# Kernel optimization log

Hardware: AMD Instinct MI355X
Metric: run time of the kernel (lower is better)

## Reference

```python
import jax, jax.numpy as jnp
import numpy as np

V = 50257; E = 1024; H = 1024; L = 256; NL = 2; D = 10


def setup_inputs() -> dict:
    key = jax.random.key(0)
    ks = jax.random.split(key, 16)
    n = lambda k, s: jax.random.normal(k, s, dtype=jnp.float32)
    return {
        "input_tok": jax.random.randint(ks[0], (1, 1), 0, V),
        "h0": n(ks[1], (NL, 1, H)),
        "c0": n(ks[2], (NL, 1, H)),
        "h_s": n(ks[3], (L, 1, H)),
        "h_t_tilde": n(ks[4], (1, 1, H)),
        "emb": n(ks[5], (V, E)) * 0.02,
        "Wp": n(ks[6], (H, H)) * (H ** -0.5),
        "wdot": n(ks[7], (1, H)) * (H ** -0.5),
        "Wbil": n(ks[8], (1, H, H)) * (H ** -0.5),
        "Wcomb": n(ks[9], (H, 2 * H)) * ((2 * H) ** -0.5),
        "bcomb": jnp.zeros((H,), jnp.float32),
        "Wih0": n(ks[10], (4 * H, E + H)) * ((E + H) ** -0.5),
        "Whh0": n(ks[11], (4 * H, H)) * (H ** -0.5),
        "bih0": jnp.zeros((4 * H,), jnp.float32),
        "bhh0": jnp.zeros((4 * H,), jnp.float32),
        "Wih1": n(ks[12], (4 * H, H)) * (H ** -0.5),
        "Whh1": n(ks[13], (4 * H, H)) * (H ** -0.5),
        "bih1": jnp.zeros((4 * H,), jnp.float32),
        "bhh1": jnp.zeros((4 * H,), jnp.float32),
        "Wout": n(ks[14], (V, H)) * (H ** -0.5),
        "bout": jnp.zeros((V,), jnp.float32),
    }


def _lstm_cell(x, h, c, Wih, Whh, bih, bhh):
    # torch LSTM gate order: i, f, g, o
    g = x @ Wih.T + bih + h @ Whh.T + bhh
    i, f, gg, o = jnp.split(g, 4, axis=-1)
    c2 = jax.nn.sigmoid(f) * c + jax.nn.sigmoid(i) * jnp.tanh(gg)
    h2 = jax.nn.sigmoid(o) * jnp.tanh(c2)
    return h2, c2


def reference(input_tok, h0, c0, h_s, h_t_tilde, emb, Wp, wdot, Wbil, Wcomb, bcomb,
              Wih0, Whh0, bih0, bhh0, Wih1, Whh1, bih1, bhh1, Wout, bout):
    embedding = emb[input_tok]                                  # [1,1,E]
    x = jnp.concatenate((embedding, h_t_tilde), axis=-1)[0]     # [1,E+H]
    h1, c1 = _lstm_cell(x, h0[0], c0[0], Wih0, Whh0, bih0, bhh0)
    h2, c2 = _lstm_cell(h1, h0[1], c0[1], Wih1, Whh1, bih1, bhh1)
    h_new = jnp.stack((h1, h2)); c_new = jnp.stack((c1, c2))
    h_t = h2                                                    # [1,H]
    Ls = h_s.shape[0]
    p_t = Ls * jax.nn.sigmoid(jnp.tanh(h_t @ Wp.T) @ wdot.T).squeeze()  # scalar
    s = jnp.round(p_t).astype(jnp.int32)
    idx = jnp.arange(Ls)
    lo = jnp.maximum(s - D, 0); hi = jnp.minimum(s + D, Ls - 1)
    mask = (idx >= lo) & (idx <= hi)                            # [L] local window
    # bilinear score h_t^T W h_s over all positions; mask outside window
    score = jnp.einsum('bh,ohk,lbk->lbo', h_t, Wbil, h_s)       # [L,1,1]
    neg = jnp.finfo(score.dtype).min
    a = jax.nn.softmax(jnp.where(mask[:, None, None], score, neg), axis=0)
    # NOTE: original uses exp(+d^2/(D/2)^2) (no minus sign); replicated faithfully.
    expo = jnp.where(mask, ((idx.astype(jnp.float32) - p_t) ** 2) / ((D / 2) ** 2), 0.0)
    a_t = a * jnp.exp(expo)[:, None, None]                      # [L,1,1]
    win = (hi - lo + 1).astype(jnp.float32)
    context = jnp.sum(a_t * h_s, axis=0, keepdims=True) / win   # [1,1,H] (mean over window)
    cat = jnp.concatenate((context, h_t[None]), axis=-1)        # [1,1,2H]
    h_t_tilde_new = jnp.tanh(cat @ Wcomb.T + bcomb)             # [1,1,H]
    y = jax.nn.log_softmax(h_t_tilde_new @ Wout.T + bout, axis=-1)  # [1,1,V]
    return (y, h_new, c_new, h_t_tilde_new, a_t, p_t)
```

## Files before the change

kernel.cpp:

```cpp
#include <hip/hip_runtime.h>
#include <math.h>

#define V 50257
#define E 1024
#define HH 1024
#define LL 256

#define O_H  (V)
#define O_C  (V + 2*HH)
#define O_HT (V + 4*HH)
#define O_A  (V + 5*HH)
#define O_P  (V + 5*HH + LL)

#define W_T    0
#define W_V    1024
#define W_CTX  2304
#define W_Z    4096
#define W_BM   54400
#define W_BS   55424

#define NB_LOGITS 786

__device__ __forceinline__ float sigmoidf_(float x) { return 1.f / (1.f + expf(-x)); }
__device__ __forceinline__ float dot4(float4 a, float4 b) {
    return a.x * b.x + a.y * b.y + a.z * b.z + a.w * b.w;
}

__device__ __forceinline__ float block_sum(float v, float* red) {
    int lane = threadIdx.x & 63, wv = threadIdx.x >> 6;
#pragma unroll
    for (int o = 32; o > 0; o >>= 1) v += __shfl_down(v, o, 64);
    if (lane == 0) red[wv] = v;
    __syncthreads();
    return red[0] + red[1] + red[2] + red[3];
}

__global__ void k_lstm(const float* __restrict__ Wih, const float* __restrict__ Whh,
                       const float* __restrict__ bih, const float* __restrict__ bhh,
                       const float* __restrict__ xa_base, const int* __restrict__ tok,
                       const float* __restrict__ xb, int na, int nb,
                       const float* __restrict__ hprev, const float* __restrict__ cprev,
                       float* __restrict__ hout, float* __restrict__ cout,
                       float* __restrict__ zero_buf) {
    const int u = blockIdx.x;
    const int K = na + nb;
    const int K4 = K >> 2, na4 = na >> 2;
    if (zero_buf && threadIdx.x == 0) zero_buf[u] = 0.f;
    const float* xa = tok ? (xa_base + (size_t)tok[0] * na) : xa_base;
    const float4* xa4 = (const float4*)xa;
    const float4* xb4 = (const float4*)xb;
    const float4* r0 = (const float4*)(Wih + (size_t)u * K);
    const float4* r1 = (const float4*)(Wih + (size_t)(u + HH) * K);
    const float4* r2 = (const float4*)(Wih + (size_t)(u + 2*HH) * K);
    const float4* r3 = (const float4*)(Wih + (size_t)(u + 3*HH) * K);
    float a0 = 0, a1 = 0, a2 = 0, a3 = 0;
    for (int j = threadIdx.x; j < K4; j += 256) {
        float4 xv = (j < na4) ? xa4[j] : xb4[j - na4];
        a0 += dot4(r0[j], xv); a1 += dot4(r1[j], xv);
        a2 += dot4(r2[j], xv); a3 += dot4(r3[j], xv);
    }
    const float4* s0 = (const float4*)(Whh + (size_t)u * HH);
    const float4* s1 = (const float4*)(Whh + (size_t)(u + HH) * HH);
    const float4* s2 = (const float4*)(Whh + (size_t)(u + 2*HH) * HH);
    const float4* s3 = (const float4*)(Whh + (size_t)(u + 3*HH) * HH);
    const float4* hp4 = (const float4*)hprev;
    {
        int j = threadIdx.x;
        float4 hv = hp4[j];
        a0 += dot4(s0[j], hv); a1 += dot4(s1[j], hv);
        a2 += dot4(s2[j], hv); a3 += dot4(s3[j], hv);
    }
    int lane = threadIdx.x & 63, wv = threadIdx.x >> 6;
#pragma unroll
    for (int o = 32; o > 0; o >>= 1) {
        a0 += __shfl_down(a0, o, 64);
        a1 += __shfl_down(a1, o, 64);
        a2 += __shfl_down(a2, o, 64);
        a3 += __shfl_down(a3, o, 64);
    }
    __shared__ float sm[4][4];
    if (lane == 0) { sm[wv][0] = a0; sm[wv][1] = a1; sm[wv][2] = a2; sm[wv][3] = a3; }
    __syncthreads();
    if (threadIdx.x == 0) {
        float gi = sm[0][0]+sm[1][0]+sm[2][0]+sm[3][0] + bih[u]        + bhh[u];
        float gf = sm[0][1]+sm[1][1]+sm[2][1]+sm[3][1] + bih[u+HH]     + bhh[u+HH];
        float gg = sm[0][2]+sm[1][2]+sm[2][2]+sm[3][2] + bih[u+2*HH]   + bhh[u+2*HH];
        float go = sm[0][3]+sm[1][3]+sm[2][3]+sm[3][3] + bih[u+3*HH]   + bhh[u+3*HH];
        float c = sigmoidf_(gf) * cprev[u] + sigmoidf_(gi) * tanhf(gg);
        hout[u] = sigmoidf_(go) * tanhf(c);
        cout[u] = c;
    }
}

__global__ void k_ptv(const float* __restrict__ Wp, const float* __restrict__ Wbil,
                      const float* __restrict__ h2, float* __restrict__ t_out,
                      float* __restrict__ v_out) {
    __shared__ float red[4];
    if (blockIdx.x < HH) {
        int r = blockIdx.x;
        const float4* row = (const float4*)(Wp + (size_t)r * HH);
        const float4* h24 = (const float4*)h2;
        float acc = dot4(row[threadIdx.x], h24[threadIdx.x]);
        float tot = block_sum(acc, red);
        if (threadIdx.x == 0) t_out[r] = tanhf(tot);
    } else {
        int b = blockIdx.x - HH;
        int h0 = b * 32;
        int k4 = threadIdx.x;
        const float4* W4 = (const float4*)Wbil;
        float4 acc = make_float4(0.f, 0.f, 0.f, 0.f);
        for (int h = h0; h < h0 + 32; ++h) {
            float hv = h2[h];
            float4 w = W4[(size_t)h * 256 + k4];
            acc.x += hv * w.x; acc.y += hv * w.y;
            acc.z += hv * w.z; acc.w += hv * w.w;
        }
        atomicAdd(&v_out[k4 * 4 + 0], acc.x);
        atomicAdd(&v_out[k4 * 4 + 1], acc.y);
        atomicAdd(&v_out[k4 * 4 + 2], acc.z);
        atomicAdd(&v_out[k4 * 4 + 3], acc.w);
    }
}

__global__ void k_attn(const float* __restrict__ wdot, const float* __restrict__ t,
                       const float* __restrict__ v, const float* __restrict__ hs,
                       float* __restrict__ ctx, float* __restrict__ a_out,
                       float* __restrict__ pt_out) {
    const int tid = threadIdx.x;
    const int lane = tid & 63, wv = tid >> 6;
    __shared__ float red[4];
    __shared__ float s_p;
    __shared__ float ssc[32];
    __shared__ float sa[LL];
    {
        const float4* w4 = (const float4*)wdot;
        const float4* t4 = (const float4*)t;
        float acc = dot4(w4[tid], t4[tid]);
        float tot = block_sum(acc, red);
        if (tid == 0) { s_p = (float)LL * sigmoidf_(tot); pt_out[0] = s_p; }
    }
    __syncthreads();
    const float p = s_p;
    const int si = (int)rintf(p);
    const int lo = max(si - 10, 0), hi = min(si + 10, LL - 1);
    const int W = hi - lo + 1;
    const float4* v4 = (const float4*)v;
    for (int l = lo + wv; l <= hi; l += 4) {
        const float4* row = (const float4*)(hs + (size_t)l * HH);
        float a = 0.f;
#pragma unroll
        for (int j = lane; j < 256; j += 64) a += dot4(row[j], v4[j]);
#pragma unroll
        for (int o = 32; o > 0; o >>= 1) a += __shfl_xor(a, o, 64);
        if (lane == 0) ssc[l - lo] = a;
    }
    __syncthreads();
    float M = -INFINITY;
    for (int i = 0; i < W; ++i) M = fmaxf(M, ssc[i]);
    float S = 0.f;
    for (int i = 0; i < W; ++i) S += expf(ssc[i] - M);
    {
        bool mask = (tid >= lo) && (tid <= hi);
        int wi = min(max(tid - lo, 0), 31);
        float e = mask ? expf(ssc[wi] - M) : 0.f;
        float d = (float)tid - p;
        float at = mask ? (e / S) * expf(d * d * 0.04f) : 0.f;
        sa[tid] = at;
        a_out[tid] = at;
    }
    __syncthreads();
    const float4* hs4 = (const float4*)hs;
    float4 c = make_float4(0.f, 0.f, 0.f, 0.f);
    for (int l = lo; l <= hi; ++l) {
        float a = sa[l];
        float4 hv = hs4[(size_t)l * 256 + tid];
        c.x += a * hv.x; c.y += a * hv.y; c.z += a * hv.z; c.w += a * hv.w;
    }
    ((float4*)ctx)[tid] = c;
}

__global__ void k_comb(const float* __restrict__ Wcomb, const float* __restrict__ bcomb,
                       const float* __restrict__ ctx, const float* __restrict__ h2,
                       const float* __restrict__ pt, float* __restrict__ outv) {
    __shared__ float red[4];
    int u = blockIdx.x;
    float p = pt[0];
    int si = (int)rintf(p);
    int lo = max(si - 10, 0), hi = min(si + 10, LL - 1);
    float inv_win = 1.f / (float)(hi - lo + 1);
    const float4* row  = (const float4*)(Wcomb + (size_t)u * (2 * HH));
    const float4* ctx4 = (const float4*)ctx;
    const float4* h24  = (const float4*)h2;
    float acc = 0;
#pragma unroll
    for (int j = threadIdx.x; j < 512; j += 256) {
        float4 xv;
        if (j < 256) {
            xv = ctx4[j];
            xv.x *= inv_win; xv.y *= inv_win; xv.z *= inv_win; xv.w *= inv_win;
        } else {
            xv = h24[j - 256];
        }
        acc += dot4(row[j], xv);
    }
    float tot = block_sum(acc, red);
    if (threadIdx.x == 0) outv[u] = tanhf(tot + bcomb[u]);
}

__global__ void k_logits(const float* __restrict__ Wout, const float* __restrict__ bout,
                         const float* __restrict__ x, float* __restrict__ z,
                         float* __restrict__ bmax, float* __restrict__ bsum) {
    const int lane = threadIdx.x & 63, wv = threadIdx.x >> 6;
    const int base = blockIdx.x * 64 + wv * 16;
    const float4* x4 = (const float4*)x;
    float4 x0 = x4[lane], x1 = x4[lane + 64], x2 = x4[lane + 128], x3 = x4[lane + 192];
    float m = -INFINITY, s = 0.f;
    if (base + 16 <= V) {
        const float4* rp = (const float4*)(Wout + (size_t)base * 1024) + lane;
        float4 c0 = rp[0], c1 = rp[64], c2 = rp[128], c3 = rp[192];
#pragma unroll
        for (int t = 0; t < 16; ++t) {
            float4 n0, n1, n2, n3;
            if (t < 15) {
                const float4* np = rp + (size_t)(t + 1) * 256;
                n0 = np[0]; n1 = np[64]; n2 = np[128]; n3 = np[192];
            }
            float acc = dot4(c0, x0) + dot4(c1, x1) + dot4(c2, x2) + dot4(c3, x3);
#pragma unroll
            for (int o = 32; o > 0; o >>= 1) acc += __shfl_xor(acc, o, 64);
            float zz = acc + bout[base + t];
            if (lane == 0) z[base + t] = zz;
            if (zz > m) { s *= expf(m - zz); m = zz; }
            s += expf(zz - m);
            c0 = n0; c1 = n1; c2 = n2; c3 = n3;
        }
    } else {
        for (int t = 0; t < 16; ++t) {
            const int r = base + t;
            if (r >= V) break;
            const float4* row = (const float4*)(Wout + (size_t)r * 1024) + lane;
            float acc = dot4(row[0], x0) + dot4(row[64], x1)
                      + dot4(row[128], x2) + dot4(row[192], x3);
#pragma unroll
            for (int o = 32; o > 0; o >>= 1) acc += __shfl_xor(acc, o, 64);
            float zz = acc + bout[r];
            if (lane == 0) z[r] = zz;
            if (zz > m) { s *= expf(m - zz); m = zz; }
            s += expf(zz - m);
        }
    }
    __shared__ float wm[4], wsv[4];
    if (lane == 0) { wm[wv] = m; wsv[wv] = s; }
    __syncthreads();
    if (threadIdx.x == 0) {
        float M = fmaxf(fmaxf(wm[0], wm[1]), fmaxf(wm[2], wm[3]));
        float S = 0.f;
        if (M != -INFINITY) {
#pragma unroll
            for (int w = 0; w < 4; ++w)
                if (wm[w] != -INFINITY) S += wsv[w] * expf(wm[w] - M);
        }
        bmax[blockIdx.x] = M; bsum[blockIdx.x] = S;
    }
}

__global__ void k_sub(const float* __restrict__ z, const float* __restrict__ bmax,
                      const float* __restrict__ bsum, int n, float* __restrict__ y) {
    int tid = threadIdx.x;
    float m = -INFINITY, s = 0.f;
    for (int i = tid; i < n; i += 256) {
        float m2 = bmax[i], s2 = bsum[i];
        float M = fmaxf(m, m2);
        if (M != -INFINITY) s = s * expf(m - M) + s2 * expf(m2 - M);
        m = M;
    }
    int lane = tid & 63, wv = tid >> 6;
#pragma unroll
    for (int o = 32; o > 0; o >>= 1) {
        float m2 = __shfl_down(m, o, 64), s2 = __shfl_down(s, o, 64);
        float M = fmaxf(m, m2);
        if (M != -INFINITY) s = s * expf(m - M) + s2 * expf(m2 - M);
        else s = 0.f;
        m = M;
    }
    __shared__ float wm[4], wsv[4];
    __shared__ float lzs;
    if (lane == 0) { wm[wv] = m; wsv[wv] = s; }
    __syncthreads();
    if (tid == 0) {
        float M = -INFINITY, S = 0.f;
#pragma unroll
        for (int w = 0; w < 4; ++w) {
            float M2 = fmaxf(M, wm[w]);
            if (M2 != -INFINITY) S = S * expf(M - M2) + wsv[w] * expf(wm[w] - M2);
            M = M2;
        }
        lzs = M + logf(S);
    }
    __syncthreads();
    float lz = lzs;
    int i = blockIdx.x * 256 + tid;
    if (i < V) y[i] = z[i] - lz;
}

extern "C" void kernel_launch(void* const* d_in, const int* in_sizes, int n_in,
                              void* d_out, int out_size, void* d_ws, size_t ws_size,
                              hipStream_t stream) {
    const int*   tok   = (const int*)  d_in[0];
    const float* h0    = (const float*)d_in[1];
    const float* c0    = (const float*)d_in[2];
    const float* hs    = (const float*)d_in[3];
    const float* htt   = (const float*)d_in[4];
    const float* emb   = (const float*)d_in[5];
    const float* Wp    = (const float*)d_in[6];
    const float* wdot  = (const float*)d_in[7];
    const float* Wbil  = (const float*)d_in[8];
    const float* Wcomb = (const float*)d_in[9];
    const float* bcomb = (const float*)d_in[10];
    const float* Wih0  = (const float*)d_in[11];
    const float* Whh0  = (const float*)d_in[12];
    const float* bih0  = (const float*)d_in[13];
    const float* bhh0  = (const float*)d_in[14];
    const float* Wih1  = (const float*)d_in[15];
    const float* Whh1  = (const float*)d_in[16];
    const float* bih1  = (const float*)d_in[17];
    const float* bhh1  = (const float*)d_in[18];
    const float* Wout  = (const float*)d_in[19];
    const float* bout  = (const float*)d_in[20];

    float* out = (float*)d_out;
    float* ws  = (float*)d_ws;

    float* h1o  = out + O_H;
    float* h2o  = out + O_H + HH;
    float* c1o  = out + O_C;
    float* c2o  = out + O_C + HH;
    float* htto = out + O_HT;
    float* ato  = out + O_A;
    float* pto  = out + O_P;

    hipLaunchKernelGGL(k_lstm, dim3(1024), dim3(256), 0, stream,
                       Wih0, Whh0, bih0, bhh0, emb, tok, htt, 1024, 1024,
                       h0, c0, h1o, c1o, ws + W_V);
    hipLaunchKernelGGL(k_lstm, dim3(1024), dim3(256), 0, stream,
                       Wih1, Whh1, bih1, bhh1, h1o, (const int*)nullptr, h1o, 1024, 0,
                       h0 + HH, c0 + HH, h2o, c2o, (float*)nullptr);
    hipLaunchKernelGGL(k_ptv, dim3(1024 + 32), dim3(256), 0, stream,
                       Wp, Wbil, h2o, ws + W_T, ws + W_V);
    hipLaunchKernelGGL(k_attn, dim3(1), dim3(256), 0, stream,
                       wdot, ws + W_T, ws + W_V, hs, ws + W_CTX, ato, pto);
    hipLaunchKernelGGL(k_comb, dim3(1024), dim3(256), 0, stream,
                       Wcomb, bcomb, ws + W_CTX, h2o, pto, htto);
    hipLaunchKernelGGL(k_logits, dim3(NB_LOGITS), dim3(256), 0, stream,
                       Wout, bout, htto, ws + W_Z, ws + W_BM, ws + W_BS);
    hipLaunchKernelGGL(k_sub, dim3((V + 255) / 256), dim3(256), 0, stream,
                       ws + W_Z, ws + W_BM, ws + W_BS, NB_LOGITS, out);
}
```

Baseline: 95.54 us.

## Fuse attention into combine kernel and stripe logits rows across waves

Merges the single-block attention kernel into the combine kernel, so each of the 1024 blocks redundantly recomputes p_t, the window scores and the context before its own Wcomb row. This removes one launch and the serialized one-block stage, at the cost of redundant reads of h_s and v in every block. The logits kernel now uses 1024 blocks whose waves stride over rows with a fixed stride, replacing 16-row contiguous chunks that had software prefetch. Hidden vectors are also copied into workspace for the later stages, and block_sum gains an extra barrier.

```diff
diff --git a/kernel.cpp b/kernel.cpp
--- a/kernel.cpp
+++ b/kernel.cpp
@@ -14,12 +14,14 @@
 
 #define W_T    0
 #define W_V    1024
-#define W_CTX  2304
+#define W_H1   2048
+#define W_H2   3072
 #define W_Z    4096
 #define W_BM   54400
 #define W_BS   55424
 
-#define NB_LOGITS 786
+#define NW   4096
+#define MAXR 13
 
 __device__ __forceinline__ float sigmoidf_(float x) { return 1.f / (1.f + expf(-x)); }
 __device__ __forceinline__ float dot4(float4 a, float4 b) {
@@ -30,6 +32,7 @@
     int lane = threadIdx.x & 63, wv = threadIdx.x >> 6;
 #pragma unroll
     for (int o = 32; o > 0; o >>= 1) v += __shfl_down(v, o, 64);
+    __syncthreads();
     if (lane == 0) red[wv] = v;
     __syncthreads();
     return red[0] + red[1] + red[2] + red[3];
@@ -41,7 +44,7 @@
                        const float* __restrict__ xb, int na, int nb,
                        const float* __restrict__ hprev, const float* __restrict__ cprev,
                        float* __restrict__ hout, float* __restrict__ cout,
-                       float* __restrict__ zero_buf) {
+                       float* __restrict__ hout2, float* __restrict__ zero_buf) {
     const int u = blockIdx.x;
     const int K = na + nb;
     const int K4 = K >> 2, na4 = na >> 2;
@@ -87,8 +90,8 @@
         float gg = sm[0][2]+sm[1][2]+sm[2][2]+sm[3][2] + bih[u+2*HH]   + bhh[u+2*HH];
         float go = sm[0][3]+sm[1][3]+sm[2][3]+sm[3][3] + bih[u+3*HH]   + bhh[u+3*HH];
         float c = sigmoidf_(gf) * cprev[u] + sigmoidf_(gi) * tanhf(gg);
-        hout[u] = sigmoidf_(go) * tanhf(c);
-        cout[u] = c;
+        float h = sigmoidf_(go) * tanhf(c);
+        hout[u] = h; cout[u] = c; hout2[u] = h;
     }
 }
 
@@ -122,25 +125,25 @@
     }
 }
 
-__global__ void k_attn(const float* __restrict__ wdot, const float* __restrict__ t,
-                       const float* __restrict__ v, const float* __restrict__ hs,
-                       float* __restrict__ ctx, float* __restrict__ a_out,
-                       float* __restrict__ pt_out) {
-    const int tid = threadIdx.x;
+__global__ void k_combattn(const float* __restrict__ wdot, const float* __restrict__ t,
+                           const float* __restrict__ v, const float* __restrict__ hs,
+                           const float* __restrict__ h2, const float* __restrict__ Wcomb,
+                           const float* __restrict__ bcomb,
+                           float* __restrict__ outv, float* __restrict__ outv2,
+                           float* __restrict__ ato, float* __restrict__ pto) {
+    const int u = blockIdx.x, tid = threadIdx.x;
     const int lane = tid & 63, wv = tid >> 6;
     __shared__ float red[4];
-    __shared__ float s_p;
     __shared__ float ssc[32];
     __shared__ float sa[LL];
+    float p;
     {
         const float4* w4 = (const float4*)wdot;
         const float4* t4 = (const float4*)t;
         float acc = dot4(w4[tid], t4[tid]);
-        float tot = block_sum(acc, red);
-        if (tid == 0) { s_p = (float)LL * sigmoidf_(tot); pt_out[0] = s_p; }
-    }
-    __syncthreads();
-    const float p = s_p;
+        p = (float)LL * sigmoidf_(block_sum(acc, red));
+    }
+    if (u == 0 && tid == 0) pto[0] = p;
     const int si = (int)rintf(p);
     const int lo = max(si - 10, 0), hi = min(si + 10, LL - 1);
     const int W = hi - lo + 1;
@@ -166,7 +169,7 @@
         float d = (float)tid - p;
         float at = mask ? (e / S) * expf(d * d * 0.04f) : 0.f;
         sa[tid] = at;
-        a_out[tid] = at;
+        if (u == 0) ato[tid] = at;
     }
     __syncthreads();
     const float4* hs4 = (const float4*)hs;
@@ -176,68 +179,31 @@
         float4 hv = hs4[(size_t)l * 256 + tid];
         c.x += a * hv.x; c.y += a * hv.y; c.z += a * hv.z; c.w += a * hv.w;
     }
-    ((float4*)ctx)[tid] = c;
-}
-
-__global__ void k_comb(const float* __restrict__ Wcomb, const float* __restrict__ bcomb,
-                       const float* __restrict__ ctx, const float* __restrict__ h2,
-                       const float* __restrict__ pt, float* __restrict__ outv) {
-    __shared__ float red[4];
-    int u = blockIdx.x;
-    float p = pt[0];
-    int si = (int)rintf(p);
-    int lo = max(si - 10, 0), hi = min(si + 10, LL - 1);
-    float inv_win = 1.f / (float)(hi - lo + 1);
-    const float4* row  = (const float4*)(Wcomb + (size_t)u * (2 * HH));
-    const float4* ctx4 = (const float4*)ctx;
-    const float4* h24  = (const float4*)h2;
-    float acc = 0;
-#pragma unroll
-    for (int j = threadIdx.x; j < 512; j += 256) {
-        float4 xv;
-        if (j < 256) {
-            xv = ctx4[j];
-            xv.x *= inv_win; xv.y *= inv_win; xv.z *= inv_win; xv.w *= inv_win;
-        } else {
-            xv = h24[j - 256];
-        }
-        acc += dot4(row[j], xv);
-    }
-    float tot = block_sum(acc, red);
-    if (threadIdx.x == 0) outv[u] = tanhf(tot + bcomb[u]);
+    const float inv_win = 1.f / (float)W;
+    c.x *= inv_win; c.y *= inv_win; c.z *= inv_win; c.w *= inv_win;
+    {
+        const float4* row = (const float4*)(Wcomb + (size_t)u * (2 * HH));
+        const float4* h24 = (const float4*)h2;
+        float acc = dot4(row[tid], c) + dot4(row[256 + tid], h24[tid]);
+        float tot = block_sum(acc, red);
+        if (tid == 0) {
+            float h = tanhf(tot + bcomb[u]);
+            outv[u] = h; outv2[u] = h;
+        }
+    }
 }
 
 __global__ void k_logits(const float* __restrict__ Wout, const float* __restrict__ bout,
                          const float* __restrict__ x, float* __restrict__ z,
                          float* __restrict__ bmax, float* __restrict__ bsum) {
-    const int lane = threadIdx.x & 63, wv = threadIdx.x >> 6;
-    const int base = blockIdx.x * 64 + wv * 16;
+    const int tid = threadIdx.x, lane = tid & 63, wvi = tid >> 6;
+    const int w = blockIdx.x * 4 + wvi;
     const float4* x4 = (const float4*)x;
     float4 x0 = x4[lane], x1 = x4[lane + 64], x2 = x4[lane + 128], x3 = x4[lane + 192];
     float m = -INFINITY, s = 0.f;
-    if (base + 16 <= V) {
-        const float4* rp = (const float4*)(Wout + (size_t)base * 1024) + lane;
-        float4 c0 = rp[0], c1 = rp[64], c2 = rp[128], c3 = rp[192];
-#pragma unroll
-        for (int t = 0; t < 16; ++t) {
-            float4 n0, n1, n2, n3;
-            if (t < 15) {
-                const float4* np = rp + (size_t)(t + 1) * 256;
-                n0 = np[0]; n1 = np[64]; n2 = np[128]; n3 = np[192];
-            }
-            float acc = dot4(c0, x0) + dot4(c1, x1) + dot4(c2, x2) + dot4(c3, x3);
-#pragma unroll
-            for (int o = 32; o > 0; o >>= 1) acc += __shfl_xor(acc, o, 64);
-            float zz = acc + bout[base + t];
-            if (lane == 0) z[base + t] = zz;
-            if (zz > m) { s *= expf(m - zz); m = zz; }
-            s += expf(zz - m);
-            c0 = n0; c1 = n1; c2 = n2; c3 = n3;
-        }
-    } else {
-        for (int t = 0; t < 16; ++t) {
-            const int r = base + t;
-            if (r >= V) break;
+    for (int i = 0; i < MAXR; ++i) {
+        int r = w + i * NW;
+        if (r < V) {
             const float4* row = (const float4*)(Wout + (size_t)r * 1024) + lane;
             float acc = dot4(row[0], x0) + dot4(row[64], x1)
                       + dot4(row[128], x2) + dot4(row[192], x3);
@@ -250,25 +216,25 @@
         }
     }
     __shared__ float wm[4], wsv[4];
-    if (lane == 0) { wm[wv] = m; wsv[wv] = s; }
-    __syncthreads();
-    if (threadIdx.x == 0) {
+    if (lane == 0) { wm[wvi] = m; wsv[wvi] = s; }
+    __syncthreads();
+    if (tid == 0) {
         float M = fmaxf(fmaxf(wm[0], wm[1]), fmaxf(wm[2], wm[3]));
         float S = 0.f;
         if (M != -INFINITY) {
 #pragma unroll
-            for (int w = 0; w < 4; ++w)
-                if (wm[w] != -INFINITY) S += wsv[w] * expf(wm[w] - M);
+            for (int q = 0; q < 4; ++q)
+                if (wm[q] != -INFINITY) S += wsv[q] * expf(wm[q] - M);
         }
         bmax[blockIdx.x] = M; bsum[blockIdx.x] = S;
     }
 }
 
 __global__ void k_sub(const float* __restrict__ z, const float* __restrict__ bmax,
-                      const float* __restrict__ bsum, int n, float* __restrict__ y) {
+                      const float* __restrict__ bsum, float* __restrict__ y) {
     int tid = threadIdx.x;
     float m = -INFINITY, s = 0.f;
-    for (int i = tid; i < n; i += 256) {
+    for (int i = tid; i < 1024; i += 256) {
         float m2 = bmax[i], s2 = bsum[i];
         float M = fmaxf(m, m2);
         if (M != -INFINITY) s = s * expf(m - M) + s2 * expf(m2 - M);
@@ -290,9 +256,9 @@
     if (tid == 0) {
         float M = -INFINITY, S = 0.f;
 #pragma unroll
-        for (int w = 0; w < 4; ++w) {
-            float M2 = fmaxf(M, wm[w]);
-            if (M2 != -INFINITY) S = S * expf(M - M2) + wsv[w] * expf(wm[w] - M2);
+        for (int q = 0; q < 4; ++q) {
+            float M2 = fmaxf(M, wm[q]);
+            if (M2 != -INFINITY) S = S * expf(M - M2) + wsv[q] * expf(wm[q] - M2);
             M = M2;
         }
         lzs = M + logf(S);
@@ -341,18 +307,18 @@
 
     hipLaunchKernelGGL(k_lstm, dim3(1024), dim3(256), 0, stream,
                        Wih0, Whh0, bih0, bhh0, emb, tok, htt, 1024, 1024,
-                       h0, c0, h1o, c1o, ws + W_V);
+                       h0, c0, h1o, c1o, ws + W_H1, ws + W_V);
     hipLaunchKernelGGL(k_lstm, dim3(1024), dim3(256), 0, stream,
-                       Wih1, Whh1, bih1, bhh1, h1o, (const int*)nullptr, h1o, 1024, 0,
-                       h0 + HH, c0 + HH, h2o, c2o, (float*)nullptr);
+                       Wih1, Whh1, bih1, bhh1, ws + W_H1, (const int*)nullptr,
+                       ws + W_H1, 1024, 0,
+                       h0 + HH, c0 + HH, h2o, c2o, ws + W_H2, (float*)nullptr);
     hipLaunchKernelGGL(k_ptv, dim3(1024 + 32), dim3(256), 0, stream,
-                       Wp, Wbil, h2o, ws + W_T, ws + W_V);
-    hipLaunchKernelGGL(k_attn, dim3(1), dim3(256), 0, stream,
-                       wdot, ws + W_T, ws + W_V, hs, ws + W_CTX, ato, pto);
-    hipLaunchKernelGGL(k_comb, dim3(1024), dim3(256), 0, stream,
-                       Wcomb, bcomb, ws + W_CTX, h2o, pto, htto);
-    hipLaunchKernelGGL(k_logits, dim3(NB_LOGITS), dim3(256), 0, stream,
-                       Wout, bout, htto, ws + W_Z, ws + W_BM, ws + W_BS);
+                       Wp, Wbil, ws + W_H2, ws + W_T, ws + W_V);
+    hipLaunchKernelGGL(k_combattn, dim3(1024), dim3(256), 0, stream,
+                       wdot, ws + W_T, ws + W_V, hs, ws + W_H2, Wcomb, bcomb,
+                       htto, ws + W_H1, ato, pto);
+    hipLaunchKernelGGL(k_logits, dim3(1024), dim3(256), 0, stream,
+                       Wout, bout, ws + W_H1, ws + W_Z, ws + W_BM, ws + W_BS);
     hipLaunchKernelGGL(k_sub, dim3((V + 255) / 256), dim3(256), 0, stream,
-                       ws + W_Z, ws + W_BM, ws + W_BS, NB_LOGITS, out);
-}
+                       ws + W_Z, ws + W_BM, ws + W_BS, out);
+}
```

Result: faster. 86.27 us (-9.7%).
